# Kernel optimization log

Measured on AMD Instinct MI355X. Metric: run time of the kernel, lower is better.

## Reference

```python
import jax, jax.numpy as jnp
import numpy as np

E = 256; D = 512; A = 5; NS = 2048; NQ = 8192; NWAY = 5
_OTHERS = np.array([[j for j in range(A) if j != i] for i in range(A)])  # [A, A-1] indices of other agents
_ROWS = np.arange(A)[:, None]


def _ln(x, g, b, eps=1e-5):
    m = x.mean(-1, keepdims=True)
    v = ((x - m) ** 2).mean(-1, keepdims=True)
    return (x - m) * jax.lax.rsqrt(v + eps) * g + b


def _mha(x, in_w, in_b, out_w, out_b, h, mask=None):
    # torch nn.MultiheadAttention (batch_first) self-attention. in_w: [3E,E], out_w: [E,E]
    B, S, Em = x.shape
    hd = Em // h
    qkv = x @ in_w.T + in_b
    q, k, v = jnp.split(qkv, 3, axis=-1)
    q = q.reshape(B, S, h, hd).transpose(0, 2, 1, 3) * (1.0 / np.sqrt(hd))
    k = k.reshape(B, S, h, hd).transpose(0, 2, 1, 3)
    v = v.reshape(B, S, h, hd).transpose(0, 2, 1, 3)
    s = jnp.einsum('bhqd,bhkd->bhqk', q, k)
    if mask is not None:
        s = jnp.where(mask, s, jnp.asarray(-1e9, s.dtype))
    a = jax.nn.softmax(s, axis=-1)
    o = jnp.einsum('bhqk,bhkd->bhqd', a, v).transpose(0, 2, 1, 3).reshape(B, S, Em)
    return o @ out_w.T + out_b


def _forward(support_x, support_y, query_x, n_way, fe0_w1, fe0_b1, fe0_g1, fe0_be1, fe0_w2, fe0_b2, fe0_g2, fe0_be2, fe1_w1, fe1_b1, fe1_g, fe1_be, fe1_w2, fe1_b2, fe2_w1, fe2_b1, fe2_w2, fe2_b2, fe2_g, fe2_be, fe3_w1, fe3_b1, fe3_w2, fe3_b2, fe3_g, fe3_be, fe4_w1, fe4_b1, fe4_w2, fe4_b2, fe4_w3, fe4_b3, msg_enc_w, msg_enc_b, agg_in_w, agg_in_b, agg_out_w, agg_out_b, proc_w1, proc_b1, proc_w2, proc_b2, internal_state, proto_in_w, proto_in_b, proto_out_w, proto_out_b, cls_w1, cls_b1, cls_w2, cls_b2, cls_w3, cls_b3, comm_w, f_w1, f_b1, f_w2, f_b2, f_w3, f_b3):
    # --- per-agent-type feature extractors (eval mode: dropout off) ---
    def fe0(x):
        h = jax.nn.relu(_ln(x @ fe0_w1 + fe0_b1, fe0_g1, fe0_be1))
        return jax.nn.relu(_ln(h @ fe0_w2 + fe0_b2, fe0_g2, fe0_be2))
    def fe1(x):
        h = jax.nn.relu(_ln(x @ fe1_w1 + fe1_b1, fe1_g, fe1_be))
        return jnp.tanh(h @ fe1_w2 + fe1_b2)
    def fe2(x):
        h = jax.nn.relu(x @ fe2_w1 + fe2_b1)
        return jax.nn.relu(_ln(h @ fe2_w2 + fe2_b2, fe2_g, fe2_be))
    def fe3(x):
        h = jax.nn.relu(x @ fe3_w1 + fe3_b1)
        return jax.nn.sigmoid(_ln(h @ fe3_w2 + fe3_b2, fe3_g, fe3_be))
    def fe4(x):
        h = jax.nn.relu(x @ fe4_w1 + fe4_b1)
        h = jax.nn.relu(h @ fe4_w2 + fe4_b2)
        return h @ fe4_w3 + fe4_b3
    feats_s = jnp.stack([fe0(support_x), fe1(support_x), fe2(support_x), fe3(support_x), fe4(support_x)])  # [A,NS,E]
    feats_q = jnp.stack([fe0(query_x), fe1(query_x), fe2(query_x), fe3(query_x), fe4(query_x)])            # [A,NQ,E]

    # --- one communication round: generate -> weight -> MHA-aggregate -> MLP-process ---
    agent_state = feats_s.mean(1) + internal_state                                         # [A,E]
    messages = jnp.tanh(jnp.einsum('ae,aef->af', agent_state, msg_enc_w) + msg_enc_b)      # [A,E]
    wgt = jax.nn.softmax(comm_w, axis=-1)                                                  # [A,A]
    msgs = messages[_OTHERS] * wgt[_ROWS, _OTHERS][..., None]                              # [A,A-1,E]
    def agg_one(m, iw, ib, ow, ob):
        return _mha(m[None], iw, ib, ow, ob, 4)[0].mean(0)
    agg = jax.vmap(agg_one)(msgs, agg_in_w, agg_in_b, agg_out_w, agg_out_b)                # [A,E]
    comb = internal_state + agg
    hh = jax.nn.relu(jnp.einsum('ae,aef->af', comb, proc_w1) + proc_b1)
    ck = jnp.einsum('ae,aef->af', hh, proc_w2) + proc_b2                                   # [A,E] communicated knowledge

    # --- class-masked prototype attention (equivalent to per-class MHA) + logits ---
    mask = support_y[:, None] == support_y[None, :]                                        # [NS,NS]
    counts = jax.ops.segment_sum(jnp.ones(support_y.shape, jnp.float32), support_y, num_segments=n_way)
    def head(fs, fq, cki, piw, pib, pw, pb, c1, c1b, c2, c2b, c3, c3b):
        att = _mha((fs + cki[None])[None], piw, pib, pw, pb, 2, mask[None, None])[0]       # [NS,E]
        psum = jax.ops.segment_sum(att, support_y, num_segments=n_way)
        protos = jnp.where(counts[:, None] > 0, psum / jnp.maximum(counts, 1.0)[:, None], 0.0)  # [n_way,E]
        eq = jnp.concatenate([fq, jnp.broadcast_to(cki, fq.shape)], axis=-1)               # [NQ,2E]
        d2 = (fq * fq).sum(-1, keepdims=True) + (protos * protos).sum(-1)[None, :] - 2.0 * (fq @ protos.T)
        dist = jnp.sqrt(jnp.maximum(d2, 1e-12))                                            # cdist
        c = jax.nn.relu(eq @ c1 + c1b)
        c = jax.nn.relu(c @ c2 + c2b)
        conf = c @ c3 + c3b                                                                # [NQ,1]
        return -dist + conf * 0.1
    logits = jax.vmap(head)(feats_s, feats_q, ck, proto_in_w, proto_in_b, proto_out_w, proto_out_b, cls_w1, cls_b1, cls_w2, cls_b2, cls_w3, cls_b3)  # [A,NQ,n_way]

    # --- decision fusion over concatenated per-agent query features ---
    qcat = feats_q.transpose(1, 0, 2).reshape(NQ, A * E)
    fh = jax.nn.relu(qcat @ f_w1 + f_b1)
    fh = jax.nn.relu(fh @ f_w2 + f_b2)
    fused = fh @ f_w3 + f_b3                                                               # [NQ,1]
    return logits, fused


def setup_inputs() -> dict:
    key = jax.random.key(0)
    ks = iter(jax.random.split(key, 80))
    def rn(shape, scale=1.0):
        return (jax.random.normal(next(ks), shape) * scale).astype(jnp.float32)
    def lin(shape, fan):
        return rn(shape, 1.0 / np.sqrt(fan))
    z = lambda s: jnp.zeros(s, jnp.float32)
    o = lambda s: jnp.ones(s, jnp.float32)
    inp = {}
    inp['support_x'] = rn((NS, D))
    inp['support_y'] = jax.random.randint(next(ks), (NS,), 0, NWAY, dtype=jnp.int32)
    inp['query_x'] = rn((NQ, D))
    inp['n_way'] = NWAY
    inp['fe0_w1'] = lin((D, 2 * E), D); inp['fe0_b1'] = z((2 * E,)); inp['fe0_g1'] = o((2 * E,)); inp['fe0_be1'] = z((2 * E,))
    inp['fe0_w2'] = lin((2 * E, E), 2 * E); inp['fe0_b2'] = z((E,)); inp['fe0_g2'] = o((E,)); inp['fe0_be2'] = z((E,))
    inp['fe1_w1'] = lin((D, E), D); inp['fe1_b1'] = z((E,)); inp['fe1_g'] = o((E,)); inp['fe1_be'] = z((E,))
    inp['fe1_w2'] = lin((E, E), E); inp['fe1_b2'] = z((E,))
    inp['fe2_w1'] = lin((D, 3 * E), D); inp['fe2_b1'] = z((3 * E,))
    inp['fe2_w2'] = lin((3 * E, E), 3 * E); inp['fe2_b2'] = z((E,)); inp['fe2_g'] = o((E,)); inp['fe2_be'] = z((E,))
    inp['fe3_w1'] = lin((D, E), D); inp['fe3_b1'] = z((E,))
    inp['fe3_w2'] = lin((E, E), E); inp['fe3_b2'] = z((E,)); inp['fe3_g'] = o((E,)); inp['fe3_be'] = z((E,))
    inp['fe4_w1'] = lin((D, 2 * E), D); inp['fe4_b1'] = z((2 * E,))
    inp['fe4_w2'] = lin((2 * E, E), 2 * E); inp['fe4_b2'] = z((E,))
    inp['fe4_w3'] = lin((E, E), E); inp['fe4_b3'] = z((E,))
    inp['msg_enc_w'] = lin((A, E, E), E); inp['msg_enc_b'] = z((A, E))
    inp['agg_in_w'] = lin((A, 3 * E, E), E); inp['agg_in_b'] = z((A, 3 * E))
    inp['agg_out_w'] = lin((A, E, E), E); inp['agg_out_b'] = z((A, E))
    inp['proc_w1'] = lin((A, E, E), E); inp['proc_b1'] = z((A, E))
    inp['proc_w2'] = lin((A, E, E), E); inp['proc_b2'] = z((A, E))
    inp['internal_state'] = rn((A, E), 0.01)
    inp['proto_in_w'] = lin((A, 3 * E, E), E); inp['proto_in_b'] = z((A, 3 * E))
    inp['proto_out_w'] = lin((A, E, E), E); inp['proto_out_b'] = z((A, E))
    inp['cls_w1'] = lin((A, 2 * E, E), 2 * E); inp['cls_b1'] = z((A, E))
    inp['cls_w2'] = lin((A, E, E // 2), E); inp['cls_b2'] = z((A, E // 2))
    inp['cls_w3'] = lin((A, E // 2, 1), E // 2); inp['cls_b3'] = z((A, 1))
    inp['comm_w'] = (jnp.eye(A) * 0.5 + 0.1).astype(jnp.float32)
    inp['f_w1'] = lin((A * E, E), A * E); inp['f_b1'] = z((E,))
    inp['f_w2'] = lin((E, E // 2), E); inp['f_b2'] = z((E // 2,))
    inp['f_w3'] = lin((E // 2, 1), E // 2); inp['f_b3'] = z((1,))
    return inp


def reference(support_x, support_y, query_x, n_way, fe0_w1, fe0_b1, fe0_g1, fe0_be1, fe0_w2, fe0_b2, fe0_g2, fe0_be2, fe1_w1, fe1_b1, fe1_g, fe1_be, fe1_w2, fe1_b2, fe2_w1, fe2_b1, fe2_w2, fe2_b2, fe2_g, fe2_be, fe3_w1, fe3_b1, fe3_w2, fe3_b2, fe3_g, fe3_be, fe4_w1, fe4_b1, fe4_w2, fe4_b2, fe4_w3, fe4_b3, msg_enc_w, msg_enc_b, agg_in_w, agg_in_b, agg_out_w, agg_out_b, proc_w1, proc_b1, proc_w2, proc_b2, internal_state, proto_in_w, proto_in_b, proto_out_w, proto_out_b, cls_w1, cls_b1, cls_w2, cls_b2, cls_w3, cls_b3, comm_w, f_w1, f_b1, f_w2, f_b2, f_w3, f_b3):
    return _forward(support_x, support_y, query_x, n_way, fe0_w1, fe0_b1, fe0_g1, fe0_be1, fe0_w2, fe0_b2, fe0_g2, fe0_be2, fe1_w1, fe1_b1, fe1_g, fe1_be, fe1_w2, fe1_b2, fe2_w1, fe2_b1, fe2_w2, fe2_b2, fe2_g, fe2_be, fe3_w1, fe3_b1, fe3_w2, fe3_b2, fe3_g, fe3_be, fe4_w1, fe4_b1, fe4_w2, fe4_b2, fe4_w3, fe4_b3, msg_enc_w, msg_enc_b, agg_in_w, agg_in_b, agg_out_w, agg_out_b, proc_w1, proc_b1, proc_w2, proc_b2, internal_state, proto_in_w, proto_in_b, proto_out_w, proto_out_b, cls_w1, cls_b1, cls_w2, cls_b2, cls_w3, cls_b3, comm_w, f_w1, f_b1, f_w2, f_b2, f_w3, f_b3)
```

## Files before the change

kernel.cpp:

```cpp
#include <hip/hip_runtime.h>
#include <hip/hip_bf16.h>

typedef __hip_bfloat16 bf16;
typedef short s8v __attribute__((ext_vector_type(8)));
typedef short s4v __attribute__((ext_vector_type(4)));
typedef float f4v __attribute__((ext_vector_type(4)));

#define A_  5
#define D_  512
#define E_  256
#define NS_ 2048
#define NQ_ 8192
#define NM_ 10240
#define NWAY_ 5
#define QSCALE 0.088388347648318447f
#define FSTR ((size_t)NM_ * E_)

__device__ inline float ldw(const void* p, size_t i, int f32) {
  return f32 ? ((const float*)p)[i] : __bfloat162float(((const bf16*)p)[i]);
}
template<bool DYN>
__device__ inline float ldT(const void* p, size_t i, int f32) {
  if (DYN) return ldw(p, i, f32);
  return ((const float*)p)[i];
// ... 20 lines not shown
__global__ void probe_k(Ptrs P, int* flags) {
  int b = blockIdx.x, lane = threadIdx.x;
  if (b == 1 || b == 3) { if (lane == 0) flags[b] = 0; return; }
  const bf16* t = (const bf16*)P.p[b];
  int n = P.sz[b];
  int K = (n >> 1) < 64 ? (n >> 1) : 64;
  bool big = false, eNZ = false, oNZ = false;
  if (lane < K) {
    float e = __bfloat162float(t[2 * lane]);
    float o = __bfloat162float(t[2 * lane + 1]);
    big = !(fabsf(e) <= 1e3f);
    eNZ = (e != 0.f); oNZ = (o != 0.f);
  }
  unsigned long long bb = __ballot(big), eb = __ballot(eNZ), ob = __ballot(oNZ);
  if (lane == 0) flags[b] = (bb != 0ull || (eb == 0ull && ob != 0ull)) ? 1 : 0;
}

__global__ void classidx_k(const int* __restrict__ y, int* __restrict__ idx,
                           int* __restrict__ cnt, int* __restrict__ cstart) {
  __shared__ int sc[NWAY_];
  int tid = threadIdx.x;
  if (tid < NWAY_) sc[tid] = 0;
  __syncthreads();
  for (int i = tid; i < NS_; i += 256) {
    int c = y[i];
    int pos = atomicAdd(&sc[c], 1);
    idx[c * NS_ + pos] = i;
  }
  __syncthreads();
  if (tid < NWAY_) cnt[tid] = sc[tid];
  if (tid == 0) { int s = 0; for (int q = 0; q < NWAY_; ++q) { cstart[q] = s; s += sc[q]; } }
}

__global__ void xcopy_k(const void* __restrict__ sx, const void* __restrict__ qx,
                        short* __restrict__ XC, const int* __restrict__ flags) {
  size_t i = ((size_t)blockIdx.x * 256 + threadIdx.x) * 4;
  const size_t SN = (size_t)NS_ * 512;
  if (i < SN) {
    int f = flags[0];
    #pragma unroll
    for (int q = 0; q < 4; ++q) XC[i + q] = f2bf(ldw(sx, i + q, f));
  } else {
    int f = flags[2];
    size_t j = i - SN;
    #pragma unroll
    for (int q = 0; q < 4; ++q) XC[i + q] = f2bf(ldw(qx, j + q, f));
  }
}

__global__ void wcat_k(Ptrs P, short* __restrict__ Wcat, float* __restrict__ bcat,
                       const int* __restrict__ flags) {
  int n = blockIdx.x * 256 + threadIdx.x;
  int k = blockIdx.y;
  int iw, ib, nl, Nloc;
  if (n < 512)       { iw = 4;  ib = 5;  nl = n;        Nloc = 512; }
  else if (n < 768)  { iw = 12; ib = 13; nl = n - 512;  Nloc = 256; }
  else if (n < 1536) { iw = 18; ib = 19; nl = n - 768;  Nloc = 768; }
  else if (n < 1792) { iw = 24; ib = 25; nl = n - 1536; Nloc = 256; }
  else               { iw = 30; ib = 31; nl = n - 1792; Nloc = 512; }
  Wcat[(size_t)n * 512 + k] = f2bf(ldw(P.p[iw], (size_t)k * Nloc + nl, flags[iw]));
  if (k == 0) bcat[n] = ldw(P.p[ib], nl, flags[ib]);
}

__global__ void wcls_k(const void* __restrict__ cw1, const void* __restrict__ fw1,
                       short* __restrict__ B2, const int* __restrict__ flags) {
  int n = blockIdx.x, a = blockIdx.y, k = threadIdx.x;
  float v;
  if (n < 256) v = ldw(cw1, ((size_t)a * 512 + k) * 256 + n, flags[51]);
  else v = ldw(fw1, ((size_t)(a * 256 + k)) * 256 + (n - 256), flags[58]);
  B2[((size_t)a * 512 + n) * 256 + k] = f2bf(v);
}

__global__ void wconv_k(Ptrs P, short* __restrict__ W2, const int* __restrict__ flags) {
  const int id = blockIdx.y;
  int src, K, N; size_t off; int tr, batch;
  switch (id) {
    case 0: src = 8;  K = 512; N = 256; off = 0;      tr = 1; batch = 1;  break;
    case 1: src = 16; K = 256; N = 256; off = 131072; tr = 1; batch = 1;  break;
    case 2: src = 20; K = 768; N = 256; off = 196608; tr = 1; batch = 1;  break;
    case 3: src = 26; K = 256; N = 256; off = 393216; tr = 1; batch = 1;  break;
    case 4: src = 32; K = 512; N = 256; off = 458752; tr = 1; batch = 1;  break;
    case 5: src = 34; K = 256; N = 256; off = 589824; tr = 1; batch = 1;  break;
    case 6: src = 53; K = 256; N = 128; off = 655360; tr = 1; batch = A_; break;
    case 7: src = 60; K = 256; N = 128; off = 819200; tr = 1; batch = 1;  break;
    default: src = 47; K = 256; N = 768; off = 851968; tr = 0; batch = A_; break;
  }
  size_t tot = (size_t)batch * K * N;
  size_t e0 = ((size_t)blockIdx.x * 256 + threadIdx.x) * 4;
  if (e0 >= tot) return;
  const void* sp = P.p[src];
  int f = flags[src];
  if (!tr) {
    #pragma unroll
    for (int q = 0; q < 4; ++q) W2[off + e0 + q] = f2bf(ldw(sp, e0 + q, f));
  } else {
    size_t kn = (size_t)K * N;
    #pragma unroll
    for (int q = 0; q < 4; ++q) {
      size_t e = e0 + q;
      int b = (int)(e / kn);
      int r = (int)(e % kn);
      int n = r / K, k = r % K;
      W2[off + e] = f2bf(ldw(sp, ((size_t)b * K + k) * N + n, f));
    }
  }
}

#define LSTR 40
template<int AMODE, int BMODE, bool DYNBIAS, bool TRB, int ACT, bool ACCUM,
         bool KSPLIT = false, bool OUTBF16 = false, bool DOMAP = false>
__global__ __launch_bounds__(256) void gemm_k(
    const void* __restrict__ A, int lda,
    const void* __restrict__ B, int ldb, size_t offB,
    const void* __restrict__ bias, size_t offBias,
    float* __restrict__ C, int ldc,
    int M, int N, int K, float alpha,
    int ia, int ib, int ibias, const int* __restrict__ flags,
    size_t sA, size_t sB, size_t sBias, size_t sC, size_t kstrideA,
    unsigned long long amap)
{
  constexpr bool GDB = (AMODE == 2) && (BMODE == 2) && TRB && !KSPLIT;
  const int fA = (AMODE == 1) ? flags[ia] : 1;
  const int fB = (BMODE == 1) ? flags[ib] : 1;
  const int fBi = DYNBIAS ? flags[ibias] : 1;
  const size_t zA = (size_t)blockIdx.z * sA;
  const size_t zB = offB + (size_t)blockIdx.z * sB;
  const size_t zBias = offBias + (size_t)blockIdx.z * sBias;
  float* Cz = C + (size_t)blockIdx.z * sC;
  bf16* Cz16 = (bf16*)C + (size_t)blockIdx.z * sC;
  const int tid = threadIdx.x;
  const int bm = blockIdx.y * 128, bn = blockIdx.x * 128;
  const int lane = tid & 63, wid = tid >> 6;
  const int lm = lane & 15, quad = lane >> 4;
  const int wy = (wid >> 1) * 64, wx = (wid & 1) * 64;
  f4v acc[4][4];
  #pragma unroll
  for (int i = 0; i < 4; ++i)
    #pragma unroll
    for (int j = 0; j < 4; ++j) acc[i][j] = (f4v)(0.f);

  if constexpr (GDB) {
    __shared__ short smem[4 * 128 * 32];
    const int srow = lane >> 2, scol = (lane & 3) * 8;
    const short* Azs = (const short*)A + zA;
    const short* Bzs = (const short*)B + zB;
    auto stage = [&](int bsel, int k0) {
      short* Asb = smem + bsel * 4096;
      short* Bsb = smem + 8192 + bsel * 4096;
      #pragma unroll
      for (int q = 0; q < 2; ++q) {
        int rb = (wid * 2 + q) * 16;
        gload16(Azs + (size_t)(bm + rb + srow) * lda + k0 + scol, Asb + rb * 32);
        gload16(Bzs + (size_t)(bn + rb + srow) * ldb + k0 + scol, Bsb + rb * 32);
      }
    };
    stage(0, 0);
    __syncthreads();
    int cur = 0;
    for (int k0 = 0; k0 < K; k0 += 32) {
      if (k0 + 32 < K) stage(cur ^ 1, k0 + 32);
      const short* Asb = smem + cur * 4096;
      const short* Bsb = smem + 8192 + cur * 4096;
      s8v af[4], bfr[4];
      #pragma unroll
      for (int mi = 0; mi < 4; ++mi)
        af[mi] = *(const s8v*)&Asb[(wy + mi*16 + lm) * 32 + quad * 8];
      #pragma unroll
      for (int ni = 0; ni < 4; ++ni)
        bfr[ni] = *(const s8v*)&Bsb[(wx + ni*16 + lm) * 32 + quad * 8];
      #pragma unroll
      for (int mi = 0; mi < 4; ++mi)
        #pragma unroll
        for (int ni = 0; ni < 4; ++ni)
          acc[mi][ni] = __builtin_amdgcn_mfma_f32_16x16x32_bf16(af[mi], bfr[ni], acc[mi][ni], 0, 0, 0);
      __syncthreads();
      cur ^= 1;
    }
  } else {
    __shared__ short As[128 * LSTR];
    __shared__ short Bs[128 * LSTR];
    const int am = tid >> 1, ah = (tid & 1) * 16;

    s8v a_s0, a_s1;
    float a_f[16];
    s8v b_s0, b_s1;
    float b_f[16];
    short b_h[16];

    auto loadA = [&](int k0) {
      int kk = k0 + ah;
      size_t base;
      if (KSPLIT) base = zA + (size_t)(kk >> 8) * kstrideA + (size_t)(bm + am) * lda + (kk & 255);
      else base = zA + (size_t)(bm + am) * lda + kk;
      if constexpr (AMODE == 2) {
        const bf16* ap = (const bf16*)A + base;
        a_s0 = *(const s8v*)ap;
        a_s1 = *(const s8v*)(ap + 8);
      } else {
        if (fA) {
          const float4* src = (const float4*)((const float*)A + base);
          #pragma unroll
          for (int q = 0; q < 4; ++q) {
            float4 v = src[q];
            a_f[q*4] = v.x; a_f[q*4+1] = v.y; a_f[q*4+2] = v.z; a_f[q*4+3] = v.w;
          }
        } else {
          #pragma unroll
          for (int q = 0; q < 16; ++q) a_f[q] = ldw(A, base + q, 0);
        }
      }
    };
    auto storeA = [&]() {
      if constexpr (AMODE == 2) {
        *(s8v*)&As[am * LSTR + ah] = a_s0;
        *(s8v*)&As[am * LSTR + ah + 8] = a_s1;
      } else {
        short tmp[16];
        #pragma unroll
        for (int q = 0; q < 16; ++q) tmp[q] = f2bf(a_f[q]);
        s4v* dst = (s4v*)&As[am * LSTR + ah];
        #pragma unroll
        for (int q = 0; q < 4; ++q) dst[q] = *(s4v*)&tmp[q*4];
      }
    };
    auto loadB = [&](int k0) {
      if constexpr (TRB) {
        int n = tid >> 1, h = (tid & 1) * 16;
        size_t base = zB + (size_t)(bn + n) * ldb + k0 + h;
        if constexpr (BMODE == 2) {
          const bf16* bp = (const bf16*)B + base;
          b_s0 = *(const s8v*)bp;
          b_s1 = *(const s8v*)(bp + 8);
        } else {
          if (fB) {
            const float4* src = (const float4*)((const float*)B + base);
            #pragma unroll
            for (int q = 0; q < 4; ++q) {
              float4 v = src[q];
              b_f[q*4] = v.x; b_f[q*4+1] = v.y; b_f[q*4+2] = v.z; b_f[q*4+3] = v.w;
            }
          } else {
            #pragma unroll
            for (int q = 0; q < 16; ++q) b_f[q] = ldw(B, base + q, 0);
          }
        }
      } else {
        int n = tid & 127, kk2 = (tid >> 7) * 16;
        #pragma unroll
        for (int j = 0; j < 16; ++j) {
          size_t bi = zB + (size_t)(k0 + kk2 + j) * ldb + bn + n;
          if constexpr (BMODE == 2) b_h[j] = ((const short*)B)[bi];
          else b_f[j] = ldT<BMODE == 1>(B, bi, fB);
        }
      }
    };
    auto storeB = [&]() {
      if constexpr (TRB) {
        int n = tid >> 1, h = (tid & 1) * 16;
        if constexpr (BMODE == 2) {
          *(s8v*)&Bs[n * LSTR + h] = b_s0;
          *(s8v*)&Bs[n * LSTR + h + 8] = b_s1;
        } else {
          short tmp[16];
          #pragma unroll
          for (int q = 0; q < 16; ++q) tmp[q] = f2bf(b_f[q]);
          s4v* dst = (s4v*)&Bs[n * LSTR + h];
          #pragma unroll
          for (int q = 0; q < 4; ++q) dst[q] = *(s4v*)&tmp[q*4];
        }
      } else {
        int n = tid & 127, kk2 = (tid >> 7) * 16;
        short tmp[16];
        #pragma unroll
        for (int j = 0; j < 16; ++j) tmp[j] = (BMODE == 2) ? b_h[j] : f2bf(b_f[j]);
        s4v* dst = (s4v*)&Bs[n * LSTR + kk2];
        #pragma unroll
        for (int q = 0; q < 4; ++q) dst[q] = *(s4v*)&tmp[q*4];
      }
    };

    loadA(0);
    loadB(0);
    for (int k0 = 0; k0 < K; k0 += 32) {
      storeA();
      storeB();
      __syncthreads();
      if (k0 + 32 < K) { loadA(k0 + 32); loadB(k0 + 32); }
      s8v af[4], bfr[4];
      #pragma unroll
      for (int mi = 0; mi < 4; ++mi)
        af[mi] = *(const s8v*)&As[(wy + mi*16 + lm) * LSTR + quad * 8];
      #pragma unroll
      for (int ni = 0; ni < 4; ++ni)
        bfr[ni] = *(const s8v*)&Bs[(wx + ni*16 + lm) * LSTR + quad * 8];
      #pragma unroll
      for (int mi = 0; mi < 4; ++mi)
        #pragma unroll
        for (int ni = 0; ni < 4; ++ni)
          acc[mi][ni] = __builtin_amdgcn_mfma_f32_16x16x32_bf16(af[mi], bfr[ni], acc[mi][ni], 0, 0, 0);
      __syncthreads();
    }
  }

  const int actc = DOMAP ? (int)((amap >> ((bn >> 7) * 2)) & 3ULL) : ACT;
  #pragma unroll
  for (int mi = 0; mi < 4; ++mi) {
    #pragma unroll
    for (int r = 0; r < 4; ++r) {
      int row = bm + wy + mi*16 + quad*4 + r;
      #pragma unroll
      for (int ni = 0; ni < 4; ++ni) {
        int col = bn + wx + ni*16 + lm;
        float v = acc[mi][ni][r] * alpha;
        if (ACCUM) v += Cz[(size_t)row * ldc + col];
        if (bias) v += ldT<DYNBIAS>(bias, zBias + col, fBi);
        if (actc == 1) v = fmaxf(v, 0.f);
        else if (actc == 2) v = tanhf(v);
        else if (actc == 3) v = 1.f / (1.f + expf(-v));
        if (OUTBF16) Cz16[(size_t)row * ldc + col] = __float2bfloat16(v);
        else Cz[(size_t)row * ldc + col] = v;
      }
    }
  }
}

template<int AMODE, int BMODE, bool DYNBIAS, bool TRB, int ACT, bool ACCUM,
         bool KSPLIT = false, bool OUTBF16 = false, bool DOMAP = false>
static void gemm(hipStream_t s, const void* A, int lda, const void* B, int ldb, size_t offB,
                 const void* bias, size_t offBias, float* C, int ldc, int M, int N, int K,
                 float alpha, int ia, int ib, int ibias, const int* flags,
                 int batch = 1, size_t sA = 0, size_t sB = 0, size_t sBias = 0, size_t sC = 0,
                 size_t kstrideA = 0, unsigned long long amap = 0) {
  dim3 g(N / 128, M / 128, batch), b(256);
  gemm_k<AMODE, BMODE, DYNBIAS, TRB, ACT, ACCUM, KSPLIT, OUTBF16, DOMAP><<<g, b, 0, s>>>(
      A, lda, B, ldb, offB, bias, offBias, C, ldc, M, N, K, alpha, ia, ib, ibias, flags,
      sA, sB, sBias, sC, kstrideA, amap);
}

template<int ACT, int W>
__global__ __launch_bounds__(256) void lnv_k(const short* __restrict__ X, const void* __restrict__ g,
                                             const void* __restrict__ be, short* __restrict__ Y,
                                             int ldx, int ldy,
                                             int ig, int ibe, const int* __restrict__ flags) {
  const int fG = flags[ig], fBe = flags[ibe];
  const int wid = threadIdx.x >> 6, lane = threadIdx.x & 63;
  const int row = blockIdx.x * 4 + wid;
  constexpr int V = W / 64;
  const short* x = X + (size_t)row * ldx + lane * V;
  float xv[V];
  if constexpr (V == 8) {
    s8v v = *(const s8v*)x;
    #pragma unroll
    for (int q = 0; q < 8; ++q) xv[q] = bf2f(v[q]);
  } else {
    s4v v = *(const s4v*)x;
    #pragma unroll
    for (int q = 0; q < 4; ++q) xv[q] = bf2f(v[q]);
  }
  float s1 = 0.f, s2 = 0.f;
  #pragma unroll
  for (int q = 0; q < V; ++q) { s1 += xv[q]; s2 += xv[q] * xv[q]; }
  #pragma unroll
  for (int o = 32; o > 0; o >>= 1) { s1 += __shfl_xor(s1, o); s2 += __shfl_xor(s2, o); }
  float mean = s1 * (1.f / W);
  float var = fmaxf(s2 * (1.f / W) - mean * mean, 0.f);
  float rstd = rsqrtf(var + 1e-5f);
  short yv[V];
  #pragma unroll
  for (int q = 0; q < V; ++q) {
    int i = lane * V + q;
    float v = (xv[q] - mean) * rstd * ldw(g, i, fG) + ldw(be, i, fBe);
    if (ACT == 1) v = fmaxf(v, 0.f);
    else if (ACT == 3) v = 1.f / (1.f + expf(-v));
    yv[q] = f2bf(v);
  }
  short* y = Y + (size_t)row * ldy + lane * V;
  if constexpr (V == 8) *(s8v*)y = *(s8v*)yv;
  else *(s4v*)y = *(s4v*)yv;
}

__global__ void statepart_k(const short* __restrict__ featsC, float* __restrict__ part) {
  int a = blockIdx.x, g = blockIdx.y, e = threadIdx.x;
  const short* p = featsC + (size_t)a * FSTR + ((size_t)g * 128) * E_ + e;
  float s = 0.f;
  for (int n = 0; n < 128; ++n) s += bf2f(p[(size_t)n * E_]);
  part[((size_t)a * 16 + g) * E_ + e] = s;
}

__global__ void statecomb_k(const float* __restrict__ part, const void* __restrict__ internal,
                            float* __restrict__ state, const int* __restrict__ flags) {
  int a = blockIdx.x, e = threadIdx.x;
  float s = 0.f;
  for (int g = 0; g < 16; ++g) s += part[((size_t)a * 16 + g) * E_ + e];
  state[a * E_ + e] = s * (1.f / NS_) + ldw(internal, (size_t)a * E_ + e, flags[46]);
}

__global__ void mvpart_k(const float* __restrict__ x, const void* __restrict__ W, int iw,
                         float* __restrict__ part, const int* __restrict__ flags) {
  int a = blockIdx.x, g = blockIdx.y, f = threadIdx.x;
  const int fW = flags[iw];
  float s = 0.f;
  size_t wb = (size_t)a * E_ * E_ + f;
  for (int e = g * 32; e < g * 32 + 32; ++e)
    s += x[a * E_ + e] * ldw(W, wb + (size_t)e * E_, fW);
  part[((size_t)a * 8 + g) * E_ + f] = s;
}

template<int ACT>
__global__ void mvcomb_k(const float* __restrict__ part, const void* __restrict__ b, int ibb,
                         float* __restrict__ y, const int* __restrict__ flags) {
  int a = blockIdx.x, f = threadIdx.x;
  float s = 0.f;
  for (int g = 0; g < 8; ++g) s += part[((size_t)a * 8 + g) * E_ + f];
  s += ldw(b, (size_t)a * E_ + f, flags[ibb]);
  if (ACT == 1) s = fmaxf(s, 0.f);
  else if (ACT == 2) s = tanhf(s);
  y[a * E_ + f] = s;
}

__device__ inline float wave_sum64(float v) {
  for (int o = 32; o > 0; o >>= 1) v += __shfl_down(v, o);
  return v;
}

__global__ __launch_bounds__(256) void qkvcomm_k(const float* __restrict__ msg,
                                                 const void* __restrict__ comm_w,
                                                 const void* __restrict__ in_w,
                                                 const void* __restrict__ in_b,
                                                 float* __restrict__ qkvc,
                                                 const int* __restrict__ flags) {
  const int fCW = flags[57], fIW = flags[38], fIB = flags[39];
  int gw = blockIdx.x * 4 + (threadIdx.x >> 6);
  int a = gw / 768, f = gw % 768;
  int lane = threadIdx.x & 63;
  float w[5]; float mx = -1e30f;
  for (int j = 0; j < 5; ++j) { w[j] = ldw(comm_w, a * 5 + j, fCW); mx = fmaxf(mx, w[j]); }
  float sum = 0.f;
  for (int j = 0; j < 5; ++j) { w[j] = __expf(w[j] - mx); sum += w[j]; }
  for (int j = 0; j < 5; ++j) w[j] /= sum;
  int others[4]; { int c = 0; for (int j = 0; j < 5; ++j) if (j != a) others[c++] = j; }
  int e0 = lane * 4;
  float4 wv;
  size_t b = (size_t)a * 768 * E_ + (size_t)f * E_ + e0;
  if (fIW) wv = *(const float4*)((const float*)in_w + b);
  else wv = make_float4(ldw(in_w, b, 0), ldw(in_w, b + 1, 0), ldw(in_w, b + 2, 0), ldw(in_w, b + 3, 0));
  float acc[4];
  #pragma unroll
  for (int t = 0; t < 4; ++t) {
    const float4 mv = *(const float4*)(msg + others[t] * E_ + e0);
    acc[t] = mv.x * wv.x + mv.y * wv.y + mv.z * wv.z + mv.w * wv.w;
  }
  #pragma unroll
  for (int t = 0; t < 4; ++t) acc[t] = wave_sum64(acc[t]);
  if (lane == 0) {
    float bb = ldw(in_b, (size_t)a * 768 + f, fIB);
    #pragma unroll
    for (int t = 0; t < 4; ++t)
      qkvc[((size_t)a * 4 + t) * 768 + f] = acc[t] * w[others[t]] + bb;
  }
}

__global__ __launch_bounds__(256) void attn4_k(const float* __restrict__ qkvc,
                                               float* __restrict__ obar) {
  int a = blockIdx.x, tid = threadIdx.x;
  __shared__ float qkv[4][768];
  __shared__ float attw[4][16];
  for (int i = tid; i < 4 * 768; i += 256) qkv[i / 768][i % 768] = qkvc[(size_t)a * 4 * 768 + i];
  __syncthreads();
  if (tid < 16) {
    int h = tid >> 2, t = tid & 3;
    float sc[4]; float mx = -1e30f;
    for (int t2 = 0; t2 < 4; ++t2) {
      float s = 0.f;
      for (int d = 0; d < 64; ++d) s += qkv[t][h * 64 + d] * qkv[t2][256 + h * 64 + d];
      sc[t2] = s * 0.125f; mx = fmaxf(mx, sc[t2]);
    }
    float ss = 0.f;
    for (int t2 = 0; t2 < 4; ++t2) { sc[t2] = __expf(sc[t2] - mx); ss += sc[t2]; }
    for (int t2 = 0; t2 < 4; ++t2) attw[h][t * 4 + t2] = sc[t2] / ss;
  }
  __syncthreads();
  {
    int e = tid, h = e >> 6;
    float s = 0.f;
    for (int t = 0; t < 4; ++t)
      for (int t2 = 0; t2 < 4; ++t2)
        s += attw[h][t * 4 + t2] * qkv[t2][512 + e];
    obar[a * E_ + e] = s * 0.25f;
  }
}

__global__ __launch_bounds__(256) void combproj_k(const float* __restrict__ obar,
                                                  const void* __restrict__ ow,
                                                  const void* __restrict__ ob,
                                                  const void* __restrict__ internal,
                                                  float* __restrict__ comb,
                                                  const int* __restrict__ flags) {
  const int fOW = flags[40], fOB = flags[41], fIN = flags[46];
  int gw = blockIdx.x * 4 + (threadIdx.x >> 6);
  int a = gw >> 8, f = gw & 255;
  int lane = threadIdx.x & 63;
  int e0 = lane * 4;
  float4 wv;
  size_t b = (size_t)a * E_ * E_ + (size_t)f * E_ + e0;
  if (fOW) wv = *(const float4*)((const float*)ow + b);
  else wv = make_float4(ldw(ow, b, 0), ldw(ow, b + 1, 0), ldw(ow, b + 2, 0), ldw(ow, b + 3, 0));
  const float4 ov = *(const float4*)(obar + a * E_ + e0);
  float s = wave_sum64(ov.x * wv.x + ov.y * wv.y + ov.z * wv.z + ov.w * wv.w);
  if (lane == 0)
    comb[a * E_ + f] = ldw(internal, (size_t)a * E_ + f, fIN) + s + ldw(ob, (size_t)a * E_ + f, fOB);
}

__global__ __launch_bounds__(256) void ckb_k(const float* __restrict__ ck,
                                             const void* __restrict__ in_w,
                                             const void* __restrict__ in_b,
                                             float* __restrict__ ckb,
                                             const int* __restrict__ flags) {
  const int fW = flags[47], fB = flags[48];
  int gw = blockIdx.x * 4 + (threadIdx.x >> 6);
  int a = gw / 768, f = gw % 768;
  int lane = threadIdx.x & 63;
  int e0 = lane * 4;
  float4 wv;
  size_t b = (size_t)a * 768 * E_ + (size_t)f * E_ + e0;
  if (fW) wv = *(const float4*)((const float*)in_w + b);
  else wv = make_float4(ldw(in_w, b, 0), ldw(in_w, b + 1, 0), ldw(in_w, b + 2, 0), ldw(in_w, b + 3, 0));
  const float4 cv = *(const float4*)(ck + a * E_ + e0);
  float s = wave_sum64(cv.x * wv.x + cv.y * wv.y + cv.z * wv.z + cv.w * wv.w);
  if (lane == 0) ckb[(size_t)a * 768 + f] = s + ldw(in_b, (size_t)a * 768 + f, fB);
}

#define LS 136
__device__ inline void stage64x128(const short* __restrict__ qkv, const int* __restrict__ myidx,
                                   int row0, int n, int ho, short* dst) {
  int t = threadIdx.x;
  int r = t >> 2, c0 = (t & 3) * 32;
  int rr = row0 + r;
  s8v v0 = (s8v)(short)0, v1 = v0, v2 = v0, v3 = v0;
  if (rr < n) {
    const s8v* s = (const s8v*)(qkv + (size_t)myidx[rr] * 768 + ho + c0);
    v0 = s[0]; v1 = s[1]; v2 = s[2]; v3 = s[3];
  }
  s8v* d = (s8v*)&dst[r * LS + c0];
  d[0] = v0; d[1] = v1; d[2] = v2; d[3] = v3;
}

__global__ __launch_bounds__(256) void attn_stats_k(
    const short* __restrict__ qkv_all, const int* __restrict__ idx,
    const int* __restrict__ cnt, const int* __restrict__ cstart,
    float* __restrict__ ml)
{
  int c = blockIdx.x, z = blockIdx.z, a = z >> 1, h = z & 1;
  int n = cnt[c];
  int r0 = blockIdx.y * 64;
  if (r0 >= n) return;
  const short* qkv = qkv_all + (size_t)a * NS_ * 768;
  const int* myidx = idx + c * NS_;
  __shared__ short Qs[64 * LS];
  __shared__ short Ks[64 * LS];
  __shared__ float Mw[4][64], Lw[4][64];
  int tid = threadIdx.x, lane = tid & 63, wid = tid >> 6;
  int lm = lane & 15, quad = lane >> 4;
  stage64x128(qkv, myidx, r0, n, h * 128, Qs);
  float m_run[16], l_run[16];
  #pragma unroll
  for (int i = 0; i < 16; ++i) { m_run[i] = -3e38f; l_run[i] = 0.f; }
  for (int j0 = 0; j0 < n; j0 += 64) {
    __syncthreads();
    stage64x128(qkv, myidx, j0, n, 256 + h * 128, Ks);
    __syncthreads();
    f4v acc[4];
    #pragma unroll
    for (int mi = 0; mi < 4; ++mi) acc[mi] = (f4v)(0.f);
    #pragma unroll
    for (int kc = 0; kc < 4; ++kc) {
      s8v bfr = *(const s8v*)&Ks[(wid * 16 + lm) * LS + kc * 32 + quad * 8];
      #pragma unroll
      for (int mi = 0; mi < 4; ++mi) {
        s8v af = *(const s8v*)&Qs[(mi * 16 + lm) * LS + kc * 32 + quad * 8];
        acc[mi] = __builtin_amdgcn_mfma_f32_16x16x32_bf16(af, bfr, acc[mi], 0, 0, 0);
      }
    }
    int col = j0 + wid * 16 + lm;
    bool cv = col < n;
    #pragma unroll
    for (int mi = 0; mi < 4; ++mi) {
      #pragma unroll
      for (int r = 0; r < 4; ++r) {
        float s = cv ? acc[mi][r] * QSCALE : -3e38f;
        float m = s;
        m = fmaxf(m, __shfl_xor(m, 1));
        m = fmaxf(m, __shfl_xor(m, 2));
        m = fmaxf(m, __shfl_xor(m, 4));
        m = fmaxf(m, __shfl_xor(m, 8));
        float p = cv ? __expf(s - m) : 0.f;
        p += __shfl_xor(p, 1); p += __shfl_xor(p, 2);
        p += __shfl_xor(p, 4); p += __shfl_xor(p, 8);
        int ri = mi * 4 + r;
        float mo = m_run[ri];
        float mn = fmaxf(mo, m);
        l_run[ri] = l_run[ri] * __expf(mo - mn) + p * __expf(m - mn);
        m_run[ri] = mn;
      }
    }
  }
  if (lm == 0) {
    #pragma unroll
    for (int mi = 0; mi < 4; ++mi)
      #pragma unroll
      for (int r = 0; r < 4; ++r) {
        int row = mi * 16 + quad * 4 + r;
        Mw[wid][row] = m_run[mi * 4 + r];
        Lw[wid][row] = l_run[mi * 4 + r];
      }
  }
  __syncthreads();
  if (tid < 64 && r0 + tid < n) {
    float m = fmaxf(fmaxf(Mw[0][tid], Mw[1][tid]), fmaxf(Mw[2][tid], Mw[3][tid]));
    float l = Lw[0][tid] * __expf(Mw[0][tid] - m) + Lw[1][tid] * __expf(Mw[1][tid] - m)
            + Lw[2][tid] * __expf(Mw[2][tid] - m) + Lw[3][tid] * __expf(Mw[3][tid] - m);
    size_t p = (size_t)z * NS_ + cstart[c] + r0 + tid;
    ml[p * 2] = m; ml[p * 2 + 1] = l;
  }
}

__global__ __launch_bounds__(256) void attn_colsum_k(
    const short* __restrict__ qkv_all, const int* __restrict__ idx,
    const int* __restrict__ cnt, const int* __restrict__ cstart,
    const float* __restrict__ ml, float* __restrict__ colsum)
{
  int c = blockIdx.x, z = blockIdx.z, a = z >> 1, h = z & 1;
  int n = cnt[c];
  int j0 = blockIdx.y * 64;
  if (j0 >= n) return;
  const short* qkv = qkv_all + (size_t)a * NS_ * 768;
  const int* myidx = idx + c * NS_;
  __shared__ short Qs[64 * LS];
  __shared__ short Ks[64 * LS];
  __shared__ float Msm[64], Lsm[64];
  int tid = threadIdx.x, lane = tid & 63, wid = tid >> 6;
  int lm = lane & 15, quad = lane >> 4;
  stage64x128(qkv, myidx, j0, n, 256 + h * 128, Ks);
  float ca = 0.f;
  for (int i0 = 0; i0 < n; i0 += 64) {
    __syncthreads();
    stage64x128(qkv, myidx, i0, n, h * 128, Qs);
    if (tid < 64) {
      int gi = i0 + tid;
      if (gi < n) {
        size_t p = (size_t)z * NS_ + cstart[c] + gi;
        Msm[tid] = ml[p * 2]; Lsm[tid] = ml[p * 2 + 1];
      } else { Msm[tid] = 0.f; Lsm[tid] = 1.f; }
    }
    __syncthreads();
    f4v acc[4];
    #pragma unroll
    for (int mi = 0; mi < 4; ++mi) acc[mi] = (f4v)(0.f);
    #pragma unroll
    for (int kc = 0; kc < 4; ++kc) {
      s8v bfr = *(const s8v*)&Ks[(wid * 16 + lm) * LS + kc * 32 + quad * 8];
      #pragma unroll
      for (int mi = 0; mi < 4; ++mi) {
        s8v af = *(const s8v*)&Qs[(mi * 16 + lm) * LS + kc * 32 + quad * 8];
        acc[mi] = __builtin_amdgcn_mfma_f32_16x16x32_bf16(af, bfr, acc[mi], 0, 0, 0);
      }
    }
    #pragma unroll
    for (int mi = 0; mi < 4; ++mi) {
      #pragma unroll
      for (int r = 0; r < 4; ++r) {
        int lrow = mi * 16 + quad * 4 + r;
        int gi = i0 + lrow;
        if (gi < n) {
          float m = Msm[lrow];
          float invl = 1.f / Lsm[lrow];
          ca += __expf(acc[mi][r] * QSCALE - m) * invl;
        }
      }
    }
  }
  ca += __shfl_xor(ca, 16);
  ca += __shfl_xor(ca, 32);
  int col = j0 + wid * 16 + lm;
  if (quad == 0 && col < n)
    colsum[(size_t)z * NS_ + cstart[c] + col] = ca;
}

#define PCH 8
__global__ __launch_bounds__(1024) void proto_reduce_k(
    const short* __restrict__ qkv_all, const int* __restrict__ idx,
    const int* __restrict__ cnt, const int* __restrict__ cstart,
    const float* __restrict__ colsum, float* __restrict__ proto_pre) {
  int c = blockIdx.x, a = blockIdx.y;
  int n = cnt[c];
  int tid = threadIdx.x, lane = tid & 63, wid = tid >> 6;
  int h = lane >> 5;
  int e0 = lane * 4;
  const short* qkv = qkv_all + (size_t)a * NS_ * 768 + 512;
  const float* csum = colsum + (size_t)(a * 2 + h) * NS_ + cstart[c];
  const int* myidx = idx + c * NS_;
  float a0 = 0.f, a1 = 0.f, a2 = 0.f, a3 = 0.f;
  for (int k = wid; k < n; k += 16) {
    float w = csum[k];
    const s4v v = *(const s4v*)(qkv + (size_t)myidx[k] * 768 + e0);
    a0 += w * bf2f(v[0]); a1 += w * bf2f(v[1]);
    a2 += w * bf2f(v[2]); a3 += w * bf2f(v[3]);
  }
  __shared__ float red[16][E_];
  *(float4*)&red[wid][e0] = make_float4(a0, a1, a2, a3);
  __syncthreads();
  if (tid < E_) {
    float s = 0.f;
    #pragma unroll
    for (int wdx = 0; wdx < 16; ++wdx) s += red[wdx][tid];
    proto_pre[((size_t)a * NWAY_ + c) * E_ + tid] = (n > 0) ? s / (float)n : 0.f;
  }
}

__global__ void proto_outproj_k(const float* __restrict__ proto_pre, const void* __restrict__ ow,
                                const void* __restrict__ ob, const int* __restrict__ cnt,
                                float* __restrict__ protos_all, float* __restrict__ pnorm,
                                const int* __restrict__ flags) {
  int c = blockIdx.x, a = blockIdx.y, e = threadIdx.x;
  const int fW = flags[49], fB = flags[50];
  __shared__ float pp[E_];
  __shared__ float r2[E_];
  pp[e] = proto_pre[((size_t)a * NWAY_ + c) * E_ + e];
  __syncthreads();
  size_t wb = (size_t)a * E_ * E_ + (size_t)e * E_;
  float s = 0.f;
  for (int k = 0; k < E_; ++k) s += pp[k] * ldw(ow, wb + k, fW);
  float v = s + ldw(ob, (size_t)a * E_ + e, fB);
  float vm = (cnt[c] > 0) ? v : 0.f;
  protos_all[((size_t)a * NWAY_ + c) * E_ + e] = vm;
  r2[e] = vm * vm;
  __syncthreads();
  for (int o = 128; o > 0; o >>= 1) { if (e < o) r2[e] += r2[e + o]; __syncthreads(); }
  if (e == 0) pnorm[a * NWAY_ + c] = r2[0];
}

__global__ void bias2_k(const float* __restrict__ ck, const void* __restrict__ w1,
                        const void* __restrict__ b1, float* __restrict__ biascat2,
                        const int* __restrict__ flags) {
  const int fW = flags[51], fB = flags[52];
  int a = blockIdx.x, n = threadIdx.x;
  __shared__ float c[E_];
  c[n] = ck[a * E_ + n]; __syncthreads();
  size_t wbase = (size_t)a * 2 * E_ * E_ + (size_t)E_ * E_ + n;
  float s = 0.f;
  for (int k = 0; k < E_; ++k) s += c[k] * ldw(w1, wbase + (size_t)k * E_, fW);
  biascat2[(size_t)a * 512 + n] = s + ldw(b1, (size_t)a * E_ + n, fB);
  biascat2[(size_t)a * 512 + 256 + n] = 0.f;
}

__global__ __launch_bounds__(256) void fcomb2_k(const short* __restrict__ U, const void* __restrict__ b1,
                                                short* __restrict__ fh1, const int* __restrict__ flags) {
  const int fB = flags[59];
  int r = threadIdx.x >> 5;
  int n0 = (threadIdx.x & 31) * 8;
  int i = blockIdx.x * 8 + r;
  float acc[8];
  #pragma unroll
  for (int q = 0; q < 8; ++q) acc[q] = ldw(b1, n0 + q, fB);
  #pragma unroll
  for (int a = 0; a < A_; ++a) {
    s8v v = *(const s8v*)(U + ((size_t)a * NQ_ + i) * 512 + 256 + n0);
    #pragma unroll
    for (int q = 0; q < 8; ++q) acc[q] += bf2f(v[q]);
  }
  short yv[8];
  #pragma unroll
  for (int q = 0; q < 8; ++q) yv[q] = f2bf(fmaxf(acc[q], 0.f));
  *(s8v*)(fh1 + (size_t)i * 256 + n0) = *(s8v*)yv;
}

__global__ __launch_bounds__(256) void logits2_k(const short* __restrict__ fqbase,
                                                 const float* __restrict__ protos_all,
                                                 const float* __restrict__ pnorm,
                                                 const bf16* __restrict__ c2all,
                                                 const void* __restrict__ w3,
                                                 const void* __restrict__ b3,
                                                 float* __restrict__ out,
                                                 const int* __restrict__ flags) {
  const int fW = flags[55], fB = flags[56];
  const int a = blockIdx.y;
  const int i = blockIdx.x * 256 + threadIdx.x;
  __shared__ float ps[NWAY_][E_];
  __shared__ float w3s[128];
  for (int t = threadIdx.x; t < NWAY_ * E_; t += 256)
    ps[t >> 8][t & 255] = protos_all[(size_t)a * NWAY_ * E_ + t];
  if (threadIdx.x < 128) w3s[threadIdx.x] = ldw(w3, (size_t)a * 128 + threadIdx.x, fW);
  __syncthreads();
  const short* fq = fqbase + (size_t)a * FSTR + (size_t)i * E_;
  float qq = 0.f, dt0 = 0.f, dt1 = 0.f, dt2 = 0.f, dt3 = 0.f, dt4 = 0.f;
  for (int e0 = 0; e0 < E_; e0 += 8) {
    s8v v = *(const s8v*)(fq + e0);
    #pragma unroll
    for (int q = 0; q < 8; ++q) {
      float x = bf2f(v[q]); int e = e0 + q;
      qq += x * x;
      dt0 += x * ps[0][e]; dt1 += x * ps[1][e]; dt2 += x * ps[2][e];
      dt3 += x * ps[3][e]; dt4 += x * ps[4][e];
    }
  }
  const short* c2 = (const short*)c2all + ((size_t)a * NQ_ + i) * 128;
  float conf = 0.f;
  for (int e0 = 0; e0 < 128; e0 += 8) {
    s8v v = *(const s8v*)(c2 + e0);
    #pragma unroll
    for (int q = 0; q < 8; ++q) conf += bf2f(v[q]) * w3s[e0 + q];
  }
  conf += ldw(b3, a, fB);
  float dts[5] = { dt0, dt1, dt2, dt3, dt4 };
  float* o = out + ((size_t)a * NQ_ + i) * NWAY_;
  #pragma unroll
  for (int c = 0; c < NWAY_; ++c) {
    float pp = pnorm[a * NWAY_ + c];
    float d2 = fmaxf(qq + pp - 2.f * dts[c], 1e-12f);
    o[c] = -sqrtf(d2) + 0.1f * conf;
  }
}

__global__ __launch_bounds__(256) void fused2_k(const float* __restrict__ h2, const void* __restrict__ w3,
                                                const void* __restrict__ b3, float* __restrict__ out,
                                                const int* __restrict__ flags) {
  const int fW = flags[62], fB = flags[63];
  int i = blockIdx.x * 256 + threadIdx.x;
  __shared__ float ws[128];
  if (threadIdx.x < 128) ws[threadIdx.x] = ldw(w3, threadIdx.x, fW);
  __syncthreads();
  const float* h = h2 + (size_t)i * 128;
  float s = 0.f;
  for (int e = 0; e < 128; e += 4) {
    float4 v = *(const float4*)(h + e);
    s += v.x * ws[e] + v.y * ws[e + 1] + v.z * ws[e + 2] + v.w * ws[e + 3];
  }
  out[i] = s + ldw(b3, 0, fB);
}

extern "C" void kernel_launch(void* const* d_in, const int* in_sizes, int n_in,
                              void* d_out, int out_size, void* d_ws, size_t ws_size,
                              hipStream_t stream) {
  (void)out_size; (void)ws_size;
  #define P(i) ((const void*)d_in[i])
  const int* support_y = (const int*)d_in[1];
  float* out = (float*)d_out;

  int* flags = (int*)d_ws;
  char* base = (char*)d_ws + 256;
  short* featsC = (short*)base;
  char* R = base + (size_t)A_ * FSTR * 2;
  short* t1cat   = (short*)R;
  short* qkv_all = (short*)R;
  short* U       = (short*)(R + (size_t)15728640);
  short* fh1     = (short*)R;
  float* fh2     = (float*)(R + (size_t)8388608);
  char* XCR = R + (size_t)57671680;
  short* XC   = (short*)XCR;
  short* tmp2 = (short*)XCR;
  short* b4   = (short*)(XCR + (size_t)NM_ * 256 * 2);
  short* clsC2_all = (short*)XCR;
  char* S = XCR + (size_t)10485760;
  float* state      = (float*)S;
  float* msg        = state + A_ * E_;
  float* ck         = msg + A_ * E_;
  float* protos_all = ck + A_ * E_;
  float* biascat2   = protos_all + A_ * NWAY_ * E_;
  float* ml         = biascat2 + A_ * 512;
  float* colsum     = ml + (size_t)A_ * 2 * NS_ * 2;
  float* proto_pre  = colsum + (size_t)A_ * 2 * NS_;
  int*   idx        = (int*)(proto_pre + A_ * NWAY_ * E_);
  int*   cnt        = idx + NWAY_ * NS_;
  int*   cstart     = cnt + NWAY_;
  float* statepart  = (float*)(cstart + NWAY_ + 3);
  float* mvp        = statepart + A_ * 16 * E_;
  float* qkvc       = mvp + A_ * 8 * E_;
  float* obar       = qkvc + A_ * 4 * 768;
  float* comb       = obar + A_ * E_;
  float* hh         = comb + A_ * E_;
  float* ckb        = hh + A_ * E_;
  float* ppart      = ckb + A_ * 768;
  float* bcat       = ppart + (size_t)A_ * NWAY_ * PCH * E_;
  short* Wcat       = (short*)(bcat + 2304);
  short* Bcat2      = Wcat + (size_t)2304 * 512;
  short* W2         = Bcat2 + (size_t)A_ * 512 * 256;

  const short* fq_base = featsC + (size_t)NS_ * E_;

  Ptrs ps;
  for (int i = 0; i < 64; ++i) {
    ps.p[i] = (i < n_in) ? d_in[i] : nullptr;
    ps.sz[i] = (i < n_in) ? in_sizes[i] : 0;
  }
  probe_k<<<64, 64, 0, stream>>>(ps, flags);
  classidx_k<<<1, 256, 0, stream>>>(support_y, idx, cnt, cstart);
  xcopy_k<<<(NM_ * 512 / 4) / 256, 256, 0, stream>>>(P(0), P(2), XC, flags);
  wcat_k<<<dim3(9, 512), 256, 0, stream>>>(ps, Wcat, bcat, flags);
  wcls_k<<<dim3(512, A_), 256, 0, stream>>>(P(51), P(58), Bcat2, flags);
  wconv_k<<<dim3(960, 9), 256, 0, stream>>>(ps, W2, flags);

  gemm<2, 2, false, true, 0, false, false, true, true>(
      stream, XC, 512, Wcat, 512, 0, bcat, 0, (float*)t1cat, 2304,
      NM_, 2304, 512, 1.f, -1, -1, -1, flags, 1, 0, 0, 0, 0, 0, 0x555555000ULL);
  lnv_k<1, 512><<<NM_ / 4, 256, 0, stream>>>(t1cat, P(6), P(7), t1cat, 2304, 2304, 6, 7, flags);
  gemm<2, 2, true, true, 0, false, false, true>(stream, t1cat, 2304, W2 + 0, 512, 0, P(9), 0,
                                                (float*)tmp2, 256, NM_, 256, 512, 1.f, -1, -1, 9, flags);
  lnv_k<1, 256><<<NM_ / 4, 256, 0, stream>>>(tmp2, P(10), P(11), featsC, 256, 256, 10, 11, flags);
  lnv_k<1, 256><<<NM_ / 4, 256, 0, stream>>>(t1cat + 512, P(14), P(15), t1cat + 512, 2304, 2304, 14, 15, flags);
  gemm<2, 2, true, true, 2, false, false, true>(stream, t1cat + 512, 2304, W2 + 131072, 256, 0, P(17), 0,
                                                (float*)(featsC + FSTR), 256, NM_, 256, 256, 1.f, -1, -1, 17, flags);
  gemm<2, 2, true, true, 0, false, false, true>(stream, t1cat + 768, 2304, W2 + 196608, 768, 0, P(21), 0,
                                                (float*)tmp2, 256, NM_, 256, 768, 1.f, -1, -1, 21, flags);
  lnv_k<1, 256><<<NM_ / 4, 256, 0, stream>>>(tmp2, P(22), P(23), featsC + 2 * FSTR, 256, 256, 22, 23, flags);
  gemm<2, 2, true, true, 0, false, false, true>(stream, t1cat + 1536, 2304, W2 + 393216, 256, 0, P(27), 0,
                                                (float*)tmp2, 256, NM_, 256, 256, 1.f, -1, -1, 27, flags);
  lnv_k<3, 256><<<NM_ / 4, 256, 0, stream>>>(tmp2, P(28), P(29), featsC + 3 * FSTR, 256, 256, 28, 29, flags);
  gemm<2, 2, true, true, 1, false, false, true>(stream, t1cat + 1792, 2304, W2 + 458752, 512, 0, P(33), 0,
                                                (float*)b4, 256, NM_, 256, 512, 1.f, -1, -1, 33, flags);
  gemm<2, 2, true, true, 0, false, false, true>(stream, b4, 256, W2 + 589824, 256, 0, P(35), 0,
                                                (float*)(featsC + 4 * FSTR), 256, NM_, 256, 256, 1.f, -1, -1, 35, flags);

  statepart_k<<<dim3(A_, 16), 256, 0, stream>>>(featsC, statepart);
  statecomb_k<<<A_, 256, 0, stream>>>(statepart, P(46), state, flags);
  mvpart_k<<<dim3(A_, 8), 256, 0, stream>>>(state, P(36), 36, mvp, flags);
  mvcomb_k<2><<<A_, 256, 0, stream>>>(mvp, P(37), 37, msg, flags);
  qkvcomm_k<<<A_ * 768 / 4, 256, 0, stream>>>(msg, P(57), P(38), P(39), qkvc, flags);
  attn4_k<<<A_, 256, 0, stream>>>(qkvc, obar);
  combproj_k<<<A_ * E_ / 4, 256, 0, stream>>>(obar, P(40), P(41), P(46), comb, flags);
  mvpart_k<<<dim3(A_, 8), 256, 0, stream>>>(comb, P(42), 42, mvp, flags);
  mvcomb_k<1><<<A_, 256, 0, stream>>>(mvp, P(43), 43, hh, flags);
  mvpart_k<<<dim3(A_, 8), 256, 0, stream>>>(hh, P(44), 44, mvp, flags);
  mvcomb_k<0><<<A_, 256, 0, stream>>>(mvp, P(45), 45, ck, flags);

  ckb_k<<<A_ * 768 / 4, 256, 0, stream>>>(ck, P(47), P(48), ckb, flags);
  gemm<2, 2, false, true, 0, false, false, true>(stream, featsC, 256, W2 + 851968, 256, 0, ckb, 0,
                                    (float*)qkv_all, 768, NS_, 768, 256, 1.f, -1, -1, -1, flags,
                                    A_, FSTR, (size_t)768 * 256, (size_t)768, (size_t)NS_ * 768);
  {
    dim3 g(NWAY_, NS_ / 64, A_ * 2);
    attn_stats_k<<<g, 256, 0, stream>>>(qkv_all, idx, cnt, cstart, ml);
    attn_colsum_k<<<g, 256, 0, stream>>>(qkv_all, idx, cnt, cstart, ml, colsum);
  }
  proto_reduce_k<<<dim3(NWAY_, A_), 1024, 0, stream>>>(qkv_all, idx, cnt, cstart, colsum, proto_pre);
  proto_outproj_k<<<dim3(NWAY_, A_), 256, 0, stream>>>(proto_pre, P(49), P(50), cnt, protos_all, ppart, flags);
  bias2_k<<<A_, 256, 0, stream>>>(ck, P(51), P(52), biascat2, flags);

  gemm<2, 2, false, true, 0, false, false, true, true>(
      stream, fq_base, 256, Bcat2, 256, 0, biascat2, 0, (float*)U, 512,
      NQ_, 512, 256, 1.f, -1, -1, -1, flags,
      A_, FSTR, (size_t)512 * 256, (size_t)512, (size_t)NQ_ * 512, 0, 0x5ULL);
  fcomb2_k<<<NQ_ / 8, 256, 0, stream>>>(U, P(59), fh1, flags);

  gemm<2, 2, true, true, 1, false, false, true>(stream, U, 512, W2 + 655360, 256, 0,
                                     P(54), 0, (float*)clsC2_all, 128, NQ_, 128, 256, 1.f, -1, -1, 54, flags,
                                     A_, (size_t)NQ_ * 512, (size_t)128 * 256, (size_t)128, (size_t)NQ_ * 128);
  logits2_k<<<dim3(NQ_ / 256, A_), 256, 0, stream>>>(fq_base, protos_all, ppart,
                                                     (const bf16*)clsC2_all, P(55), P(56), out, flags);

  gemm<2, 2, true, true, 1, false>(stream, fh1, 256, W2 + 819200, 256, 0, P(61), 0, fh2, 128,
                                   NQ_, 128, 256, 1.f, -1, -1, 61, flags);
  fused2_k<<<NQ_ / 256, 256, 0, stream>>>(fh2, P(62), P(63), out + (size_t)A_ * NQ_ * NWAY_, flags);
}
```

Baseline: 841.4 us.

## Add 128x256-tile double-buffered GEMM kernel for the three widest projections

Adds a new 512-thread GEMM kernel with a 128x256 output tile and double-buffered shared-memory staging, so the load of the next K slice overlaps the MFMA work on the current one. It is used for the concatenated first-layer projection, the batched QKV projection and the query classifier projection, all of which have wide N. The goal is more reuse of each A tile and fewer pipeline stalls per K step, at the cost of doubled shared memory and fewer blocks per launch. The activation-map lookup is now indexed per wave column (bn+wx), so a 256-wide tile can apply different activations to its two 128-column halves.

Result: no change. 841.9 us (+0.1%).

```diff
diff --git a/kernel.cpp b/kernel.cpp
--- a/kernel.cpp
+++ b/kernel.cpp
@@ -346,7 +346,7 @@
     }
   }
 
-  const int actc = DOMAP ? (int)((amap >> ((bn >> 7) * 2)) & 3ULL) : ACT;
+  const int actc = DOMAP ? (int)((amap >> (((bn + wx) >> 7) * 2)) & 3ULL) : ACT;
   #pragma unroll
   for (int mi = 0; mi < 4; ++mi) {
     #pragma unroll
@@ -379,6 +379,102 @@
   gemm_k<AMODE, BMODE, DYNBIAS, TRB, ACT, ACCUM, KSPLIT, OUTBF16, DOMAP><<<g, b, 0, s>>>(
       A, lda, B, ldb, offB, bias, offBias, C, ldc, M, N, K, alpha, ia, ib, ibias, flags,
       sA, sB, sBias, sC, kstrideA, amap);
+}
+
+template<bool DYNBIAS, int ACT, bool OUTBF16, bool DOMAP>
+__global__ __launch_bounds__(512) void gemmw_k(
+    const short* __restrict__ A, int lda,
+    const short* __restrict__ B, int ldb,
+    const void* __restrict__ bias,
+    float* __restrict__ C, int ldc,
+    int M, int N, int K,
+    int ibias, const int* __restrict__ flags,
+    size_t sA, size_t sB, size_t sBias, size_t sC,
+    unsigned long long amap)
+{
+  const int fBi = DYNBIAS ? flags[ibias] : 1;
+  const short* Az = A + (size_t)blockIdx.z * sA;
+  const short* Bz = B + (size_t)blockIdx.z * sB;
+  const size_t zBias = (size_t)blockIdx.z * sBias;
+  float* Cz = C + (size_t)blockIdx.z * sC;
+  bf16* Cz16 = (bf16*)C + (size_t)blockIdx.z * sC;
+  __shared__ short smem[2 * 4096 + 2 * 8192];
+  const int tid = threadIdx.x;
+  const int bm = blockIdx.y * 128, bn = blockIdx.x * 256;
+  const int lane = tid & 63, wid = tid >> 6;
+  const int lm = lane & 15, quad = lane >> 4;
+  const int wy = (wid >> 2) * 64, wx = (wid & 3) * 64;
+  const int srow = lane >> 2, scol = (lane & 3) * 8;
+  f4v acc[4][4];
+  #pragma unroll
+  for (int i = 0; i < 4; ++i)
+    #pragma unroll
+    for (int j = 0; j < 4; ++j) acc[i][j] = (f4v)(0.f);
+
+  auto stage = [&](int bsel, int k0) {
+    short* Asb = smem + bsel * 4096;
+    short* Bsb = smem + 8192 + bsel * 8192;
+    int ra = wid * 16;
+    gload16(Az + (size_t)(bm + ra + srow) * lda + k0 + scol, Asb + ra * 32);
+    #pragma unroll
+    for (int q = 0; q < 2; ++q) {
+      int rb = wid * 32 + q * 16;
+      gload16(Bz + (size_t)(bn + rb + srow) * ldb + k0 + scol, Bsb + rb * 32);
+    }
+  };
+  stage(0, 0);
+  __syncthreads();
+  int cur = 0;
+  for (int k0 = 0; k0 < K; k0 += 32) {
+    if (k0 + 32 < K) stage(cur ^ 1, k0 + 32);
+    const short* Asb = smem + cur * 4096;
+    const short* Bsb = smem + 8192 + cur * 8192;
+    s8v af[4], bfr[4];
+    #pragma unroll
+    for (int mi = 0; mi < 4; ++mi)
+      af[mi] = *(const s8v*)&Asb[(wy + mi*16 + lm) * 32 + quad * 8];
+    #pragma unroll
+    for (int ni = 0; ni < 4; ++ni)
+      bfr[ni] = *(const s8v*)&Bsb[(wx + ni*16 + lm) * 32 + quad * 8];
+    #pragma unroll
+    for (int mi = 0; mi < 4; ++mi)
+      #pragma unroll
+      for (int ni = 0; ni < 4; ++ni)
+        acc[mi][ni] = __builtin_amdgcn_mfma_f32_16x16x32_bf16(af[mi], bfr[ni], acc[mi][ni], 0, 0, 0);
+    __syncthreads();
+    cur ^= 1;
+  }
+
+  const int actc = DOMAP ? (int)((amap >> (((bn + wx) >> 7) * 2)) & 3ULL) : ACT;
+  #pragma unroll
+  for (int mi = 0; mi < 4; ++mi) {
+    #pragma unroll
+    for (int r = 0; r < 4; ++r) {
+      int row = bm + wy + mi*16 + quad*4 + r;
+      #pragma unroll
+      for (int ni = 0; ni < 4; ++ni) {
+        int col = bn + wx + ni*16 + lm;
+        float v = acc[mi][ni][r];
+        if (bias) v += ldT<DYNBIAS>(bias, zBias + col, fBi);
+        if (actc == 1) v = fmaxf(v, 0.f);
+        else if (actc == 2) v = tanhf(v);
+        else if (actc == 3) v = 1.f / (1.f + expf(-v));
+        if (OUTBF16) Cz16[(size_t)row * ldc + col] = __float2bfloat16(v);
+        else Cz[(size_t)row * ldc + col] = v;
+      }
+    }
+  }
+}
+
+template<bool DYNBIAS, int ACT, bool OUTBF16, bool DOMAP = false>
+static void gemmw(hipStream_t s, const short* A, int lda, const short* B, int ldb,
+                  const void* bias, float* C, int ldc, int M, int N, int K,
+                  int ibias, const int* flags, int batch = 1,
+                  size_t sA = 0, size_t sB = 0, size_t sBias = 0, size_t sC = 0,
+                  unsigned long long amap = 0) {
+  dim3 g(N / 256, M / 128, batch), b(512);
+  gemmw_k<DYNBIAS, ACT, OUTBF16, DOMAP><<<g, b, 0, s>>>(
+      A, lda, B, ldb, bias, C, ldc, M, N, K, ibias, flags, sA, sB, sBias, sC, amap);
 }
 
 template<int ACT, int W>
@@ -943,9 +1039,8 @@
   wcls_k<<<dim3(512, A_), 256, 0, stream>>>(P(51), P(58), Bcat2, flags);
   wconv_k<<<dim3(960, 9), 256, 0, stream>>>(ps, W2, flags);
 
-  gemm<2, 2, false, true, 0, false, false, true, true>(
-      stream, XC, 512, Wcat, 512, 0, bcat, 0, (float*)t1cat, 2304,
-      NM_, 2304, 512, 1.f, -1, -1, -1, flags, 1, 0, 0, 0, 0, 0, 0x555555000ULL);
+  gemmw<false, 0, true, true>(stream, XC, 512, Wcat, 512, bcat, (float*)t1cat, 2304,
+                              NM_, 2304, 512, -1, flags, 1, 0, 0, 0, 0, 0x555555000ULL);
   lnv_k<1, 512><<<NM_ / 4, 256, 0, stream>>>(t1cat, P(6), P(7), t1cat, 2304, 2304, 6, 7, flags);
   gemm<2, 2, true, true, 0, false, false, true>(stream, t1cat, 2304, W2 + 0, 512, 0, P(9), 0,
                                                 (float*)tmp2, 256, NM_, 256, 512, 1.f, -1, -1, 9, flags);
@@ -977,9 +1072,9 @@
   mvcomb_k<0><<<A_, 256, 0, stream>>>(mvp, P(45), 45, ck, flags);
 
   ckb_k<<<A_ * 768 / 4, 256, 0, stream>>>(ck, P(47), P(48), ckb, flags);
-  gemm<2, 2, false, true, 0, false, false, true>(stream, featsC, 256, W2 + 851968, 256, 0, ckb, 0,
-                                    (float*)qkv_all, 768, NS_, 768, 256, 1.f, -1, -1, -1, flags,
-                                    A_, FSTR, (size_t)768 * 256, (size_t)768, (size_t)NS_ * 768);
+  gemmw<false, 0, true>(stream, featsC, 256, W2 + 851968, 256, ckb, (float*)qkv_all, 768,
+                        NS_, 768, 256, -1, flags,
+                        A_, FSTR, (size_t)768 * 256, (size_t)768, (size_t)NS_ * 768);
   {
     dim3 g(NWAY_, NS_ / 64, A_ * 2);
     attn_stats_k<<<g, 256, 0, stream>>>(qkv_all, idx, cnt, cstart, ml);
@@ -989,10 +1084,9 @@
   proto_outproj_k<<<dim3(NWAY_, A_), 256, 0, stream>>>(proto_pre, P(49), P(50), cnt, protos_all, ppart, flags);
   bias2_k<<<A_, 256, 0, stream>>>(ck, P(51), P(52), biascat2, flags);
 
-  gemm<2, 2, false, true, 0, false, false, true, true>(
-      stream, fq_base, 256, Bcat2, 256, 0, biascat2, 0, (float*)U, 512,
-      NQ_, 512, 256, 1.f, -1, -1, -1, flags,
-      A_, FSTR, (size_t)512 * 256, (size_t)512, (size_t)NQ_ * 512, 0, 0x5ULL);
+  gemmw<false, 0, true, true>(stream, fq_base, 256, Bcat2, 256, biascat2, (float*)U, 512,
+                              NQ_, 512, 256, -1, flags,
+                              A_, FSTR, (size_t)512 * 256, (size_t)512, (size_t)NQ_ * 512, 0x5ULL);
   fcomb2_k<<<NQ_ / 8, 256, 0, stream>>>(U, P(59), fh1, flags);
 
   gemm<2, 2, true, true, 1, false, false, true>(stream, U, 512, W2 + 655360, 256, 0,
```
